# Kernel tuning notes

Hardware: AMD Instinct MI355X
Metric: run time of the kernel (lower is better)

## Reference

```python
import jax, jax.numpy as jnp
import numpy as np

B, C, S = 4, 512, 8192   # batch, channels, seq len
E = 256                  # q_dim // r1 = projected dim
D = 256                  # dilaion: block size; window width = 2*D (D even)


def setup_inputs() -> dict:
    key = jax.random.key(0)
    ks = jax.random.split(key, 6)
    w = 0.05
    return {
        "x1": jax.random.normal(ks[0], (B, C, S), jnp.float32),
        "mask": jnp.ones((B, 1, S), jnp.float32),
        "Wq": jax.random.normal(ks[1], (E, C), jnp.float32) * w,
        "bq": jnp.zeros((E,), jnp.float32),
        "Wk": jax.random.normal(ks[2], (E, C), jnp.float32) * w,
        "bk": jnp.zeros((E,), jnp.float32),
        "Wv": jax.random.normal(ks[3], (E, C), jnp.float32) * w,
        "bv": jnp.zeros((E,), jnp.float32),
        "Wo": jax.random.normal(ks[4], (C, E), jnp.float32) * w,
        "bo": jnp.zeros((C,), jnp.float32),
    }


def _windows(x, nb, d):
    # x: [B, ch, S] -> nb overlapping windows of width 2d (stride d, halo d//2 each side)
    b, ch, _ = x.shape
    xp = jnp.pad(x, ((0, 0), (0, 0), (d // 2, d // 2)))  # [B, ch, S + d]
    lo = xp[:, :, : nb * d].reshape(b, ch, nb, d)
    hi = xp[:, :, d:].reshape(b, ch, nb, d)
    return jnp.concatenate([lo, hi], axis=-1).transpose(0, 2, 1, 3)  # [B, nb, ch, 2d]


def reference(x1, mask, Wq, bq, Wk, bk, Wv, bv, Wo, bo):
    nb = S // D  # S divisible by D -> no tail padding branch
    # 1x1 conv projections
    q = jnp.einsum('ec,bcs->bes', Wq, x1) + bq[None, :, None]
    k = jnp.einsum('ec,bcs->bes', Wk, x1) + bk[None, :, None]
    v = jnp.einsum('ec,bcs->bes', Wv, x1) + bv[None, :, None]

    qw = q.reshape(B, E, nb, D).transpose(0, 2, 1, 3)   # [B, nb, E, D]
    kw = _windows(k, nb, D)                              # [B, nb, E, 2D]
    vw = _windows(v, nb, D)                              # [B, nb, E, 2D]
    pm = mask[:, 0:1, :]                                 # padding mask [B,1,S]
    pmw = _windows(pm, nb, D)                            # [B, nb, 1, 2D]

    W = 2 * D
    # original loop `window_mask[:, :, i:i+D] = 1 for i in range(D)` -> union covers
    # columns [0, 2D-2]; only the last column stays 0 (rows identical)
    win = (jnp.arange(W) < W - 1).astype(jnp.float32)    # [2D]
    fmask = win[None, None, None, :] * pmw               # [B, nb, 1, 2D]

    energy = jnp.einsum('bneq,bnek->bnqk', qw, kw) / np.float32(np.sqrt(E))
    attn = jax.nn.softmax(energy + jnp.log(fmask + 1e-6), axis=-1) * fmask
    out = jnp.einsum('bnek,bnqk->bneq', vw, attn)        # [B, nb, E, D]

    h = jax.nn.gelu(out, approximate=False)
    h = jnp.einsum('oe,bneq->bnoq', Wo, h) + bo[None, None, :, None]  # [B, nb, C, D]
    y = h.transpose(0, 2, 1, 3).reshape(B, C, nb * D)[:, :, :S]
    return y * mask[:, 0:1, :]
```

## Files before the change

### kernel.cpp

```cpp
#include <hip/hip_runtime.h>
#include <hip/hip_bf16.h>

typedef __attribute__((ext_vector_type(8))) short short8;
typedef __attribute__((ext_vector_type(4))) float f32x4;
typedef __attribute__((ext_vector_type(4))) int int4v;

#define DI __device__ __forceinline__

constexpr int Bq = 4, Cc = 512, Ss = 8192, Ee = 256;
constexpr int SP = 8448;
constexpr long XSLAB = 4194304;

DI unsigned short f2bf(float f) {
    unsigned int u = __float_as_uint(f);
    unsigned int r = u + 0x7fffu + ((u >> 16) & 1u);
    return (unsigned short)(r >> 16);
}

union U16x8 { int4v v; unsigned short u[8]; };

DI void gll16(const void* g, void* l) {
    __builtin_amdgcn_global_load_lds(
        (const __attribute__((address_space(1))) unsigned int*)g,
        (__attribute__((address_space(3))) unsigned int*)l, 16, 0, 0);
}

DI unsigned pkbf(float lo, float hi) {
    unsigned r;
    asm("v_cvt_pk_bf16_f32 %0, %1, %2" : "=v"(r) : "v"(lo), "v"(hi));
    return r;
}

DI short8 mk8(unsigned a, unsigned b, unsigned c, unsigned d) {
    int4v v; v[0] = (int)a; v[1] = (int)b; v[2] = (int)c; v[3] = (int)d;
    union { int4v i; short8 s; } U; U.i = v; return U.s;
}

DI f32x4 max4(f32x4 a, f32x4 b) {
    f32x4 r;
    r[0] = fmaxf(a[0], b[0]); r[1] = fmaxf(a[1], b[1]);
    r[2] = fmaxf(a[2], b[2]); r[3] = fmaxf(a[3], b[3]);
    return r;
}

DI float gelu_t(float x) {
    float x2 = x * x;
    float z = x * (0.7978845608f + 0.0356774081f * x2);
    float az = fabsf(z);
    float e = __expf(-2.f * az);
    float th = (1.f - e) / (1.f + e);
    th = (z < 0.f) ? -th : th;
    return 0.5f * x * (1.f + th);
}

DI int SIG(int k)  { return ((k & 4) << 2) | ((k & 24) >> 1) | (k & 3); }
DI int SIG2(int k) { return SIG(SIG(k)); }

__global__ __launch_bounds__(256) void kprep(
    const float* __restrict__ Wq, const float* __restrict__ Wk, const float* __restrict__ Wv,
    const float* __restrict__ Wo, unsigned short* __restrict__ Wqkv_b, unsigned short* __restrict__ Wo_b,
    unsigned short* __restrict__ kTp, unsigned short* __restrict__ vp)
{
    int blk = blockIdx.x, t = threadIdx.x;
    if (blk < 1536) {
        int i = blk * 256 + t;
        if (i < 768 * 512) {
            int m = i >> 9, c = i & 511;
            const float* src = (m < 256) ? Wq : ((m < 512) ? Wk : Wv);
            Wqkv_b[i] = f2bf(src[(m & 255) * 512 + c]);
        }
        if (i < 512 * 256) {
            int kap = i & 255;
            int src = (i & ~255) | (kap & ~31) | SIG(kap & 31);
            Wo_b[i] = f2bf(Wo[src]);
        }
    } else {
        int i = (blk - 1536) * 256 + t;
        int4v z = {0, 0, 0, 0};
        if (i < 32768) {
            int b = i >> 13, r = i & 8191;
            int side = r >> 12, off = r & 4095;
            *(int4v*)(kTp + (long)b * SP * 256 + (long)(side ? 8320 : 0) * 256 + off * 8) = z;
        } else {
            int j = i - 32768;
            int b = j >> 13, r = j & 8191;
            int row = r >> 5, side = (r >> 4) & 1, sc = r & 15;
            *(int4v*)(vp + ((long)b * 256 + row) * SP + side * 8320 + sc * 8) = z;
        }
    }
}

__global__ __launch_bounds__(256) void ktr_x(const float* __restrict__ x1g, unsigned short* __restrict__ xT4)
{
    const float* x1b = x1g + (long)blockIdx.y * Cc * Ss;
    unsigned short* xT = xT4 + (long)blockIdx.y * XSLAB;
    __shared__ unsigned short tile[64][72];
    int t = threadIdx.x;
    int bs = blockIdx.x & 127, bc = blockIdx.x >> 7;
    int s0 = bs * 64, c0 = bc * 64;
    int cl = t >> 4, sl = (t & 15) * 4;
    for (int it = 0; it < 4; ++it) {
        int c = cl + it * 16;
        float4 vv = *(const float4*)(x1b + (long)(c0 + c) * Ss + s0 + sl);
        tile[c][sl + 0] = f2bf(vv.x);
        tile[c][sl + 1] = f2bf(vv.y);
        tile[c][sl + 2] = f2bf(vv.z);
        tile[c][sl + 3] = f2bf(vv.w);
    }
    __syncthreads();
    int s_loc = t >> 2, cseg = (t & 3) * 16;
    for (int half = 0; half < 2; ++half) {
        U16x8 u;
        for (int j = 0; j < 8; ++j) u.u[j] = tile[cseg + half * 8 + j][s_loc];
        *(int4v*)(xT + (long)(s0 + s_loc) * Cc + c0 + cseg + half * 8) = u.v;
    }
}

__global__ __launch_bounds__(256) void kqkv(
    const unsigned short* __restrict__ xT4, const unsigned short* __restrict__ Wqkv,
    const float* __restrict__ bq, const float* __restrict__ bk, const float* __restrict__ bv,
    unsigned short* __restrict__ qT, unsigned short* __restrict__ kTp, unsigned short* __restrict__ vp,
    int b0)
{
    __shared__ int4v As[1024], Bs[1024];
    int b = b0 + blockIdx.y;
    const unsigned short* xT = xT4 + (long)blockIdx.y * XSLAB;
    int wg = blockIdx.x;
    int type = wg >> 7, id = wg & 127;
    const unsigned short *A, *Bt; unsigned short* Op;
    long opitch; const float* bias; bool biasRow;
    if (type < 2) {
        int mt = id >> 1, nt = id & 1;
        A  = xT + (long)(mt * 128) * 512;
        Bt = Wqkv + (long)(type * 256 + nt * 128) * 512;
        if (type == 0)
            Op = qT + (long)b * Ss * Ee + (long)(mt * 128) * Ee + nt * 128;
        else
            Op = kTp + (long)b * SP * Ee + (long)(128 + mt * 128) * Ee + nt * 128;
        opitch = Ee;
        bias = (type ? bk : bq) + nt * 128;
        biasRow = false;
    } else {
        int mt = id >> 6, nt = id & 63;
        A  = Wqkv + (long)(512 + mt * 128) * 512;
        Bt = xT + (long)(nt * 128) * 512;
        Op = vp + (long)b * Ee * SP + (long)(mt * 128) * SP + 128 + nt * 128;
        opitch = SP;
        bias = bv + mt * 128;
        biasRow = true;
    }
    int t = threadIdx.x, lane = t & 63, wv = t >> 6;
    int wr = (wv >> 1) * 64, wc = (wv & 1) * 64;

    int soff[4];
    #pragma unroll
    for (int i = 0; i < 4; ++i) {
        int seg = t + 256 * i, row = seg >> 3, cs = seg & 7;
        soff[i] = row * 512 + ((cs ^ (row & 7)) * 8);
    }
    char* adst = (char*)As + wv * 1024;
    char* bdst = (char*)Bs + wv * 1024;

    f32x4 acc[4][4] = {};
    for (int kk = 0; kk < 8; ++kk) {
        #pragma unroll
        for (int i = 0; i < 4; ++i) {
            gll16(A  + soff[i] + kk * 64, adst + i * 4096);
            gll16(Bt + soff[i] + kk * 64, bdst + i * 4096);
        }
        asm volatile("s_waitcnt vmcnt(0)" ::: "memory");
        __syncthreads();
        for (int ks = 0; ks < 2; ++ks) {
            int csk = ks * 4 + (lane >> 4);
            short8 af[4], bfr[4];
            #pragma unroll
            for (int mi = 0; mi < 4; ++mi) {
                int m = wr + mi * 16 + (lane & 15);
                af[mi] = *(const short8*)&As[m * 8 + (csk ^ (m & 7))];
            }
            #pragma unroll
            for (int ni = 0; ni < 4; ++ni) {
                int nn = wc + ni * 16 + (lane & 15);
                bfr[ni] = *(const short8*)&Bs[nn * 8 + (csk ^ (nn & 7))];
            }
            #pragma unroll
            for (int mi = 0; mi < 4; ++mi)
                #pragma unroll
                for (int ni = 0; ni < 4; ++ni)
                    acc[mi][ni] = __builtin_amdgcn_mfma_f32_16x16x32_bf16(af[mi], bfr[ni], acc[mi][ni], 0, 0, 0);
        }
        __syncthreads();
    }
    for (int mi = 0; mi < 4; ++mi)
        for (int ni = 0; ni < 4; ++ni) {
            int mrow = wr + mi * 16 + ((lane >> 4) * 4);
            int ncol = wc + ni * 16 + (lane & 15);
            int nc2 = biasRow ? ((ncol & ~31) | SIG2(ncol & 31)) : ncol;
            for (int r = 0; r < 4; ++r) {
                float bval = biasRow ? bias[mrow + r] : bias[ncol];
                Op[(long)(mrow + r) * opitch + nc2] = f2bf(acc[mi][ni][r] + bval);
            }
        }
}

__global__ __launch_bounds__(512, 1) void kattn(
    const unsigned short* __restrict__ qT, const unsigned short* __restrict__ kTp,
    const unsigned short* __restrict__ vp,  const unsigned short* __restrict__ Wo_b,
    const float* __restrict__ mask, const float* __restrict__ bo,
    float* __restrict__ y)
{
    __shared__ __align__(16) char SH[137216];
    float* fmaskL = (float*)(SH + 131072);
    float* lmaskL = (float*)(SH + 133120);
    float* boL    = (float*)(SH + 135168);

    int t = threadIdx.x, lane = t & 63, wv = t >> 6;
    int G = lane >> 4, l15 = lane & 15;

    int phys = blockIdx.x;
    int xx = phys & 7, kk2 = phys >> 3;
    int L = ((xx + 8 * (kk2 >> 1)) << 1) | (kk2 & 1);
    int qh = L & 1, n = (L >> 1) & 31, b = L >> 6;
    int sqw = n * 256 + qh * 128 + wv * 16;

    short8 qfrag[8];
    #pragma unroll
    for (int s = 0; s < 8; ++s)
        qfrag[s] = *(const short8*)(qT + ((long)b * Ss + sqw + l15) * 256 + 32 * s + 8 * G);

    {
        int i = t;
        int sw = n * 256 - 128 + i;
        float f = 0.f;
        if (i != 511 && sw >= 0 && sw < Ss) f = mask[(long)b * Ss + sw];
        fmaskL[i] = f;
        lmaskL[i] = __logf(f + 1e-6f);
    }
    if (t < 128) ((float4*)boL)[t] = ((const float4*)bo)[t];

    const unsigned short* ksrcp[4];
    const unsigned short* vsrcp[4];
    #pragma unroll
    for (int i = 0; i < 4; ++i) {
        int krow = wv * 8 + i * 2 + (lane >> 5);
        ksrcp[i] = kTp + ((long)b * SP + n * 256 + krow) * 256 + (((lane & 31) ^ (krow & 7)) * 8);
        int erow = wv * 32 + i * 8 + (lane >> 3);
        vsrcp[i] = vp + ((long)b * 256 + erow) * SP + n * 256 + (((lane & 7) ^ ((lane >> 3) & 7)) * 8);
    }

#define STAGE(CH, BUF) {                                                      \
        char* kl = SH + (BUF) * 32768 + wv * 4096;                            \
        char* vl = SH + 65536 + (BUF) * 32768 + wv * 4096;                    \
        _Pragma("unroll")                                                     \
        for (int i = 0; i < 4; ++i) gll16(ksrcp[i] + (long)(CH) * 16384, kl + i * 1024); \
        _Pragma("unroll")                                                     \
        for (int i = 0; i < 4; ++i) gll16(vsrcp[i] + (CH) * 64, vl + i * 1024);          \
    }

    STAGE(0, 0)
    STAGE(1, 1)
    asm volatile("s_waitcnt vmcnt(8) lgkmcnt(0)" ::: "memory");
    __builtin_amdgcn_s_barrier();

    float mrun = -1e30f, lrun = 0.f;
    f32x4 oacc[16] = {};

    for (int ch = 0; ch < 8; ++ch) {
        const char* KB = SH + (ch & 1) * 32768;
        const char* VB = SH + 65536 + (ch & 1) * 32768;

        f32x4 eacc[4] = {};
        __builtin_amdgcn_s_setprio(1);
        #pragma unroll
        for (int s = 0; s < 8; ++s) {
            short8 kf[4];
            #pragma unroll
            for (int tt = 0; tt < 4; ++tt)
                kf[tt] = *(const short8*)(KB + (16 * tt + l15) * 512 + (((4 * s + G) ^ (l15 & 7)) * 16));
            #pragma unroll
            for (int tt = 0; tt < 4; ++tt)
                eacc[tt] = __builtin_amdgcn_mfma_f32_16x16x32_bf16(kf[tt], qfrag[s], eacc[tt], 0, 0, 0);
        }
        __builtin_amdgcn_s_setprio(0);

        int w0 = ch * 64;
        f32x4 lm[4], fm[4];
        #pragma unroll
        for (int tt = 0; tt < 4; ++tt) {
            lm[tt] = *(const f32x4*)&lmaskL[w0 + 16 * tt + 4 * G];
            fm[tt] = *(const f32x4*)&fmaskL[w0 + 16 * tt + 4 * G];
        }

        f32x4 ev[4];
        f32x4 m4;
        #pragma unroll
        for (int tt = 0; tt < 4; ++tt) {
            ev[tt] = eacc[tt] * 0.0625f + lm[tt];
            m4 = tt ? max4(m4, ev[tt]) : ev[tt];
        }
        float cm = fmaxf(fmaxf(m4[0], m4[1]), fmaxf(m4[2], m4[3]));
        cm = fmaxf(cm, __shfl_xor(cm, 16));
        cm = fmaxf(cm, __shfl_xor(cm, 32));
        if (__any(cm > mrun + 8.f)) {
            float mn = fmaxf(mrun, cm);
            float sc = __expf(mrun - mn);
            mrun = mn; lrun *= sc;
            #pragma unroll
            for (int et = 0; et < 16; ++et) oacc[et] *= sc;
        }

        unsigned pc[8];
        float ssum = 0.f;
        #pragma unroll
        for (int tt = 0; tt < 4; ++tt) {
            f32x4 p;
            p[0] = __expf(ev[tt][0] - mrun);
            p[1] = __expf(ev[tt][1] - mrun);
            p[2] = __expf(ev[tt][2] - mrun);
            p[3] = __expf(ev[tt][3] - mrun);
            ssum += (p[0] + p[1]) + (p[2] + p[3]);
            f32x4 pf = p * fm[tt];
            pc[2 * tt]     = pkbf(pf[0], pf[1]);
            pc[2 * tt + 1] = pkbf(pf[2], pf[3]);
        }
        ssum += __shfl_xor(ssum, 16);
        ssum += __shfl_xor(ssum, 32);
        lrun += ssum;

        __builtin_amdgcn_s_setprio(1);
        #pragma unroll
        for (int s = 0; s < 2; ++s) {
            short8 pf = mk8(pc[4 * s], pc[4 * s + 1], pc[4 * s + 2], pc[4 * s + 3]);
            #pragma unroll
            for (int et = 0; et < 16; ++et) {
                short8 vf = *(const short8*)(VB + (16 * et + l15) * 128 + (((4 * s + G) ^ (l15 & 7)) * 16));
                oacc[et] = __builtin_amdgcn_mfma_f32_16x16x32_bf16(vf, pf, oacc[et], 0, 0, 0);
            }
        }
        __builtin_amdgcn_s_setprio(0);

        asm volatile("s_waitcnt lgkmcnt(0)" ::: "memory");
        __builtin_amdgcn_s_barrier();
        if (ch < 6) {
            STAGE(ch + 2, ch & 1)
            asm volatile("s_waitcnt vmcnt(8)" ::: "memory");
        } else if (ch == 6) {
            asm volatile("s_waitcnt vmcnt(0)" ::: "memory");
        }
        __builtin_amdgcn_s_barrier();
    }

    float linv = 1.f / lrun;
    unsigned hc[32];
    #pragma unroll
    for (int et = 0; et < 16; ++et) {
        f32x4 xv = oacc[et] * linv;
        hc[2 * et]     = pkbf(gelu_t(xv[0]), gelu_t(xv[1]));
        hc[2 * et + 1] = pkbf(gelu_t(xv[2]), gelu_t(xv[3]));
    }
    float ym = fmaskL[128 + qh * 128 + wv * 16 + l15];

    const unsigned short* wsrcp[4];
    #pragma unroll
    for (int i = 0; i < 4; ++i) {
        int wrow = wv * 8 + i * 2 + (lane >> 5);
        wsrcp[i] = Wo_b + (long)wrow * 256 + (((lane & 31) ^ (wrow & 7)) * 8);
    }
#define WSTAGE(ST, BUF) {                                                     \
        char* wl = SH + (BUF) * 32768 + wv * 4096;                            \
        _Pragma("unroll")                                                     \
        for (int i = 0; i < 4; ++i) gll16(wsrcp[i] + (ST) * 16384, wl + i * 1024); \
    }

    WSTAGE(0, 0)
    WSTAGE(1, 1)
    asm volatile("s_waitcnt vmcnt(4)" ::: "memory");
    __builtin_amdgcn_s_barrier();

    for (int step = 0; step < 8; ++step) {
        const char* WB = SH + (step & 1) * 32768;
        __builtin_amdgcn_s_setprio(1);
        #pragma unroll
        for (int otl = 0; otl < 4; ++otl) {
            f32x4 pacc = {};
            #pragma unroll
            for (int s = 0; s < 8; ++s) {
                short8 wf = *(const short8*)(WB + (16 * otl + l15) * 512 + (((4 * s + G) ^ (l15 & 7)) * 16));
                short8 hs = mk8(hc[4 * s], hc[4 * s + 1], hc[4 * s + 2], hc[4 * s + 3]);
                pacc = __builtin_amdgcn_mfma_f32_16x16x32_bf16(wf, hs, pacc, 0, 0, 0);
            }
            int o0 = step * 64 + 16 * otl + 4 * G;
            f32x4 bo4 = *(const f32x4*)&boL[o0];
            #pragma unroll
            for (int r = 0; r < 4; ++r)
                y[((long)b * Cc + o0 + r) * Ss + sqw + l15] = (pacc[r] + bo4[r]) * ym;
        }
        __builtin_amdgcn_s_setprio(0);
        asm volatile("s_waitcnt lgkmcnt(0)" ::: "memory");
        __builtin_amdgcn_s_barrier();
        if (step < 6) {
            WSTAGE(step + 2, step & 1)
            asm volatile("s_waitcnt vmcnt(4)" ::: "memory");
        } else if (step == 6) {
            asm volatile("s_waitcnt vmcnt(0)" ::: "memory");
        }
        __builtin_amdgcn_s_barrier();
    }
#undef STAGE
#undef WSTAGE
}

extern "C" void kernel_launch(void* const* d_in, const int* in_sizes, int n_in,
                              void* d_out, int out_size, void* d_ws, size_t ws_size,
                              hipStream_t stream)
{
    const float* x1   = (const float*)d_in[0];
    const float* mask = (const float*)d_in[1];
    const float* Wq   = (const float*)d_in[2];
    const float* bq   = (const float*)d_in[3];
    const float* Wk   = (const float*)d_in[4];
    const float* bk   = (const float*)d_in[5];
    const float* Wv   = (const float*)d_in[6];
    const float* bv   = (const float*)d_in[7];
    const float* Wo   = (const float*)d_in[8];
    const float* bo   = (const float*)d_in[9];
    float* y = (float*)d_out;

    if (ws_size < 60817408u) return;
    char* w = (char*)d_ws;
    unsigned short* Wqkv_b = (unsigned short*)(w);
    unsigned short* Wo_b   = (unsigned short*)(w + 786432);
    unsigned short* qT     = (unsigned short*)(w + 1048576);
    unsigned short* kTp    = (unsigned short*)(w + 17825792);
    unsigned short* vp     = (unsigned short*)(w + 35127296);
    unsigned short* xT4    = (unsigned short*)(w + 52428800);

    int g = (int)((ws_size - 52428800u) / 8388608u);
    if (g < 1) g = 1;
    if (g > 4) g = 4;

    kprep<<<1792, 256, 0, stream>>>(Wq, Wk, Wv, Wo, Wqkv_b, Wo_b, kTp, vp);
    for (int b0 = 0; b0 < 4; b0 += g) {
        int gy = (4 - b0 < g) ? (4 - b0) : g;
        ktr_x<<<dim3(1024, gy), 256, 0, stream>>>(x1 + (long)b0 * Cc * Ss, xT4);
        kqkv<<<dim3(384, gy), 256, 0, stream>>>(xT4, Wqkv_b, bq, bk, bv, qT, kTp, vp, b0);
    }
    kattn<<<256, 512, 0, stream>>>(qT, kTp, vp, Wo_b, mask, bo, y);
}
```

Before: 118.9 us.

## Software-pipeline QK^T one chunk ahead and switch softmax to exp2

Computes the QK energy MFMA block for chunk ch+1 before the softmax and PV work of chunk ch, so matrix ops can overlap the exp/max reductions. The K+V staging wait is tightened (vmcnt 8 to 4) so the next chunk's K is ready earlier. The softmax moves to base 2 by folding log2(e) into the scale and storing the mask log in base 2, which avoids an extra multiply per exp. It costs a second set of energy accumulators, which raises register pressure, and the waits become stricter.

```diff
diff --git a/kernel.cpp b/kernel.cpp
--- a/kernel.cpp
+++ b/kernel.cpp
@@ -211,7 +211,7 @@
 {
     __shared__ __align__(16) char SH[137216];
     float* fmaskL = (float*)(SH + 131072);
-    float* lmaskL = (float*)(SH + 133120);
+    float* l2maskL = (float*)(SH + 133120);
     float* boL    = (float*)(SH + 135168);
 
     int t = threadIdx.x, lane = t & 63, wv = t >> 6;
@@ -234,7 +234,7 @@
         float f = 0.f;
         if (i != 511 && sw >= 0 && sw < Ss) f = mask[(long)b * Ss + sw];
         fmaskL[i] = f;
-        lmaskL[i] = __logf(f + 1e-6f);
+        l2maskL[i] = __log2f(f + 1e-6f);
     }
     if (t < 128) ((float4*)boL)[t] = ((const float4*)bo)[t];
 
@@ -257,37 +257,46 @@
         for (int i = 0; i < 4; ++i) gll16(vsrcp[i] + (CH) * 64, vl + i * 1024);          \
     }
 
+#define QKBLOCK(E, KB) {                                                      \
+        __builtin_amdgcn_s_setprio(1);                                        \
+        _Pragma("unroll")                                                     \
+        for (int s = 0; s < 8; ++s) {                                         \
+            short8 kf[4];                                                     \
+            _Pragma("unroll")                                                 \
+            for (int tt = 0; tt < 4; ++tt)                                    \
+                kf[tt] = *(const short8*)((KB) + (16 * tt + l15) * 512 + (((4 * s + G) ^ (l15 & 7)) * 16)); \
+            _Pragma("unroll")                                                 \
+            for (int tt = 0; tt < 4; ++tt)                                    \
+                E[tt] = __builtin_amdgcn_mfma_f32_16x16x32_bf16(kf[tt], qfrag[s], E[tt], 0, 0, 0); \
+        }                                                                     \
+        __builtin_amdgcn_s_setprio(0);                                        \
+    }
+
     STAGE(0, 0)
     STAGE(1, 1)
-    asm volatile("s_waitcnt vmcnt(8) lgkmcnt(0)" ::: "memory");
+    asm volatile("s_waitcnt vmcnt(4) lgkmcnt(0)" ::: "memory");
     __builtin_amdgcn_s_barrier();
 
     float mrun = -1e30f, lrun = 0.f;
     f32x4 oacc[16] = {};
-
+    f32x4 eC[4] = {}, eN[4] = {};
+
+    QKBLOCK(eC, SH)
+
+    #pragma unroll 2
     for (int ch = 0; ch < 8; ++ch) {
-        const char* KB = SH + (ch & 1) * 32768;
         const char* VB = SH + 65536 + (ch & 1) * 32768;
 
-        f32x4 eacc[4] = {};
-        __builtin_amdgcn_s_setprio(1);
-        #pragma unroll
-        for (int s = 0; s < 8; ++s) {
-            short8 kf[4];
-            #pragma unroll
-            for (int tt = 0; tt < 4; ++tt)
-                kf[tt] = *(const short8*)(KB + (16 * tt + l15) * 512 + (((4 * s + G) ^ (l15 & 7)) * 16));
-            #pragma unroll
-            for (int tt = 0; tt < 4; ++tt)
-                eacc[tt] = __builtin_amdgcn_mfma_f32_16x16x32_bf16(kf[tt], qfrag[s], eacc[tt], 0, 0, 0);
-        }
-        __builtin_amdgcn_s_setprio(0);
+        if (ch < 7) {
+            const char* KBn = SH + ((ch + 1) & 1) * 32768;
+            QKBLOCK(eN, KBn)
+        }
 
         int w0 = ch * 64;
         f32x4 lm[4], fm[4];
         #pragma unroll
         for (int tt = 0; tt < 4; ++tt) {
-            lm[tt] = *(const f32x4*)&lmaskL[w0 + 16 * tt + 4 * G];
+            lm[tt] = *(const f32x4*)&l2maskL[w0 + 16 * tt + 4 * G];
             fm[tt] = *(const f32x4*)&fmaskL[w0 + 16 * tt + 4 * G];
         }
 
@@ -295,15 +304,15 @@
         f32x4 m4;
         #pragma unroll
         for (int tt = 0; tt < 4; ++tt) {
-            ev[tt] = eacc[tt] * 0.0625f + lm[tt];
+            ev[tt] = eC[tt] * 0.09016844f + lm[tt];
             m4 = tt ? max4(m4, ev[tt]) : ev[tt];
         }
         float cm = fmaxf(fmaxf(m4[0], m4[1]), fmaxf(m4[2], m4[3]));
         cm = fmaxf(cm, __shfl_xor(cm, 16));
         cm = fmaxf(cm, __shfl_xor(cm, 32));
-        if (__any(cm > mrun + 8.f)) {
+        if (__any(cm > mrun + 11.5416f)) {
             float mn = fmaxf(mrun, cm);
-            float sc = __expf(mrun - mn);
+            float sc = exp2f(mrun - mn);
             mrun = mn; lrun *= sc;
             #pragma unroll
             for (int et = 0; et < 16; ++et) oacc[et] *= sc;
@@ -314,10 +323,10 @@
         #pragma unroll
         for (int tt = 0; tt < 4; ++tt) {
             f32x4 p;
-            p[0] = __expf(ev[tt][0] - mrun);
-            p[1] = __expf(ev[tt][1] - mrun);
-            p[2] = __expf(ev[tt][2] - mrun);
-            p[3] = __expf(ev[tt][3] - mrun);
+            p[0] = exp2f(ev[tt][0] - mrun);
+            p[1] = exp2f(ev[tt][1] - mrun);
+            p[2] = exp2f(ev[tt][2] - mrun);
+            p[3] = exp2f(ev[tt][3] - mrun);
             ssum += (p[0] + p[1]) + (p[2] + p[3]);
             f32x4 pf = p * fm[tt];
             pc[2 * tt]     = pkbf(pf[0], pf[1]);
@@ -343,11 +352,14 @@
         __builtin_amdgcn_s_barrier();
         if (ch < 6) {
             STAGE(ch + 2, ch & 1)
-            asm volatile("s_waitcnt vmcnt(8)" ::: "memory");
+            asm volatile("s_waitcnt vmcnt(4)" ::: "memory");
         } else if (ch == 6) {
             asm volatile("s_waitcnt vmcnt(0)" ::: "memory");
         }
         __builtin_amdgcn_s_barrier();
+
+        #pragma unroll
+        for (int tt = 0; tt < 4; ++tt) { eC[tt] = eN[tt]; eN[tt] = (f32x4){}; }
     }
 
     float linv = 1.f / lrun;
@@ -408,6 +420,7 @@
     }
 #undef STAGE
 #undef WSTAGE
+#undef QKBLOCK
 }
 
 extern "C" void kernel_launch(void* const* d_in, const int* in_sizes, int n_in,
```

New measurement: 122.8 us. 1.03x slower.

## Fuse x transpose into prep kernel, stage xT in output buffer, use exp2 softmax

Applied to the files above, without the earlier changes.

Merges the x1 bf16 transpose into the weight-prep kernel and launches a single qkv GEMM over all batches, storing the transposed activations in the output buffer instead of a workspace slab. This removes several kernel launches and the batch-group loop. Softmax now works in base 2 with a folded scale and log2 mask, so exp2 replaces __expf, and the first Wo tile is prefetched during the last attention chunk. Reusing d_out as scratch depends on kattn fully overwriting y after kqkv has finished reading xT, which stream ordering provides.

```diff
diff --git a/kernel.cpp b/kernel.cpp
--- a/kernel.cpp
+++ b/kernel.cpp
@@ -56,14 +56,39 @@
 DI int SIG(int k)  { return ((k & 4) << 2) | ((k & 24) >> 1) | (k & 3); }
 DI int SIG2(int k) { return SIG(SIG(k)); }
 
-__global__ __launch_bounds__(256) void kprep(
+__global__ __launch_bounds__(256) void kpre(
+    const float* __restrict__ x1,
     const float* __restrict__ Wq, const float* __restrict__ Wk, const float* __restrict__ Wv,
     const float* __restrict__ Wo, unsigned short* __restrict__ Wqkv_b, unsigned short* __restrict__ Wo_b,
-    unsigned short* __restrict__ kTp, unsigned short* __restrict__ vp)
+    unsigned short* __restrict__ kTp, unsigned short* __restrict__ vp,
+    unsigned short* __restrict__ xTo)
 {
     int blk = blockIdx.x, t = threadIdx.x;
-    if (blk < 1536) {
-        int i = blk * 256 + t;
+    if (blk < 4096) {
+        int bb = blk >> 10, inner = blk & 1023;
+        const float* x1b = x1 + (long)bb * Cc * Ss;
+        unsigned short* xT = xTo + (long)bb * XSLAB;
+        __shared__ unsigned short tile[64][72];
+        int bs = inner & 127, bc = inner >> 7;
+        int s0 = bs * 64, c0 = bc * 64;
+        int cl = t >> 4, sl = (t & 15) * 4;
+        for (int it = 0; it < 4; ++it) {
+            int c = cl + it * 16;
+            float4 vv = *(const float4*)(x1b + (long)(c0 + c) * Ss + s0 + sl);
+            tile[c][sl + 0] = f2bf(vv.x);
+            tile[c][sl + 1] = f2bf(vv.y);
+            tile[c][sl + 2] = f2bf(vv.z);
+            tile[c][sl + 3] = f2bf(vv.w);
+        }
+        __syncthreads();
+        int s_loc = t >> 2, cseg = (t & 3) * 16;
+        for (int half = 0; half < 2; ++half) {
+            U16x8 u;
+            for (int j = 0; j < 8; ++j) u.u[j] = tile[cseg + half * 8 + j][s_loc];
+            *(int4v*)(xT + (long)(s0 + s_loc) * Cc + c0 + cseg + half * 8) = u.v;
+        }
+    } else if (blk < 5632) {
+        int i = (blk - 4096) * 256 + t;
         if (i < 768 * 512) {
             int m = i >> 9, c = i & 511;
             const float* src = (m < 256) ? Wq : ((m < 512) ? Wk : Wv);
@@ -75,7 +100,7 @@
             Wo_b[i] = f2bf(Wo[src]);
         }
     } else {
-        int i = (blk - 1536) * 256 + t;
+        int i = (blk - 5632) * 256 + t;
         int4v z = {0, 0, 0, 0};
         if (i < 32768) {
             int b = i >> 13, r = i & 8191;
@@ -90,41 +115,14 @@
     }
 }
 
-__global__ __launch_bounds__(256) void ktr_x(const float* __restrict__ x1g, unsigned short* __restrict__ xT4)
-{
-    const float* x1b = x1g + (long)blockIdx.y * Cc * Ss;
-    unsigned short* xT = xT4 + (long)blockIdx.y * XSLAB;
-    __shared__ unsigned short tile[64][72];
-    int t = threadIdx.x;
-    int bs = blockIdx.x & 127, bc = blockIdx.x >> 7;
-    int s0 = bs * 64, c0 = bc * 64;
-    int cl = t >> 4, sl = (t & 15) * 4;
-    for (int it = 0; it < 4; ++it) {
-        int c = cl + it * 16;
-        float4 vv = *(const float4*)(x1b + (long)(c0 + c) * Ss + s0 + sl);
-        tile[c][sl + 0] = f2bf(vv.x);
-        tile[c][sl + 1] = f2bf(vv.y);
-        tile[c][sl + 2] = f2bf(vv.z);
-        tile[c][sl + 3] = f2bf(vv.w);
-    }
-    __syncthreads();
-    int s_loc = t >> 2, cseg = (t & 3) * 16;
-    for (int half = 0; half < 2; ++half) {
-        U16x8 u;
-        for (int j = 0; j < 8; ++j) u.u[j] = tile[cseg + half * 8 + j][s_loc];
-        *(int4v*)(xT + (long)(s0 + s_loc) * Cc + c0 + cseg + half * 8) = u.v;
-    }
-}
-
 __global__ __launch_bounds__(256) void kqkv(
     const unsigned short* __restrict__ xT4, const unsigned short* __restrict__ Wqkv,
     const float* __restrict__ bq, const float* __restrict__ bk, const float* __restrict__ bv,
-    unsigned short* __restrict__ qT, unsigned short* __restrict__ kTp, unsigned short* __restrict__ vp,
-    int b0)
+    unsigned short* __restrict__ qT, unsigned short* __restrict__ kTp, unsigned short* __restrict__ vp)
 {
     __shared__ int4v As[1024], Bs[1024];
-    int b = b0 + blockIdx.y;
-    const unsigned short* xT = xT4 + (long)blockIdx.y * XSLAB;
+    int b = blockIdx.y;
+    const unsigned short* xT = xT4 + (long)b * XSLAB;
     int wg = blockIdx.x;
     int type = wg >> 7, id = wg & 127;
     const unsigned short *A, *Bt; unsigned short* Op;
@@ -210,9 +208,9 @@
     float* __restrict__ y)
 {
     __shared__ __align__(16) char SH[137216];
-    float* fmaskL = (float*)(SH + 131072);
-    float* lmaskL = (float*)(SH + 133120);
-    float* boL    = (float*)(SH + 135168);
+    float* fmaskL  = (float*)(SH + 131072);
+    float* l2maskL = (float*)(SH + 133120);
+    float* boL     = (float*)(SH + 135168);
 
     int t = threadIdx.x, lane = t & 63, wv = t >> 6;
     int G = lane >> 4, l15 = lane & 15;
@@ -234,7 +232,7 @@
         float f = 0.f;
         if (i != 511 && sw >= 0 && sw < Ss) f = mask[(long)b * Ss + sw];
         fmaskL[i] = f;
-        lmaskL[i] = __logf(f + 1e-6f);
+        l2maskL[i] = __log2f(f + 1e-6f);
     }
     if (t < 128) ((float4*)boL)[t] = ((const float4*)bo)[t];
 
@@ -247,6 +245,12 @@
         int erow = wv * 32 + i * 8 + (lane >> 3);
         vsrcp[i] = vp + ((long)b * 256 + erow) * SP + n * 256 + (((lane & 7) ^ ((lane >> 3) & 7)) * 8);
     }
+    const unsigned short* wsrcp[4];
+    #pragma unroll
+    for (int i = 0; i < 4; ++i) {
+        int wrow = wv * 8 + i * 2 + (lane >> 5);
+        wsrcp[i] = Wo_b + (long)wrow * 256 + (((lane & 31) ^ (wrow & 7)) * 8);
+    }
 
 #define STAGE(CH, BUF) {                                                      \
         char* kl = SH + (BUF) * 32768 + wv * 4096;                            \
@@ -256,6 +260,11 @@
         _Pragma("unroll")                                                     \
         for (int i = 0; i < 4; ++i) gll16(vsrcp[i] + (CH) * 64, vl + i * 1024);          \
     }
+#define WSTAGE(ST, BUF) {                                                     \
+        char* wl = SH + (BUF) * 32768 + wv * 4096;                            \
+        _Pragma("unroll")                                                     \
+        for (int i = 0; i < 4; ++i) gll16(wsrcp[i] + (ST) * 16384, wl + i * 1024); \
+    }
 
     STAGE(0, 0)
     STAGE(1, 1)
@@ -287,7 +296,7 @@
         f32x4 lm[4], fm[4];
         #pragma unroll
         for (int tt = 0; tt < 4; ++tt) {
-            lm[tt] = *(const f32x4*)&lmaskL[w0 + 16 * tt + 4 * G];
+            lm[tt] = *(const f32x4*)&l2maskL[w0 + 16 * tt + 4 * G];
             fm[tt] = *(const f32x4*)&fmaskL[w0 + 16 * tt + 4 * G];
         }
 
@@ -295,15 +304,15 @@
         f32x4 m4;
         #pragma unroll
         for (int tt = 0; tt < 4; ++tt) {
-            ev[tt] = eacc[tt] * 0.0625f + lm[tt];
+            ev[tt] = eacc[tt] * 0.09016844f + lm[tt];
             m4 = tt ? max4(m4, ev[tt]) : ev[tt];
         }
         float cm = fmaxf(fmaxf(m4[0], m4[1]), fmaxf(m4[2], m4[3]));
         cm = fmaxf(cm, __shfl_xor(cm, 16));
         cm = fmaxf(cm, __shfl_xor(cm, 32));
-        if (__any(cm > mrun + 8.f)) {
+        if (__any(cm > mrun + 11.5416f)) {
             float mn = fmaxf(mrun, cm);
-            float sc = __expf(mrun - mn);
+            float sc = exp2f(mrun - mn);
             mrun = mn; lrun *= sc;
             #pragma unroll
             for (int et = 0; et < 16; ++et) oacc[et] *= sc;
@@ -314,10 +323,10 @@
         #pragma unroll
         for (int tt = 0; tt < 4; ++tt) {
             f32x4 p;
-            p[0] = __expf(ev[tt][0] - mrun);
-            p[1] = __expf(ev[tt][1] - mrun);
-            p[2] = __expf(ev[tt][2] - mrun);
-            p[3] = __expf(ev[tt][3] - mrun);
+            p[0] = exp2f(ev[tt][0] - mrun);
+            p[1] = exp2f(ev[tt][1] - mrun);
+            p[2] = exp2f(ev[tt][2] - mrun);
+            p[3] = exp2f(ev[tt][3] - mrun);
             ssum += (p[0] + p[1]) + (p[2] + p[3]);
             f32x4 pf = p * fm[tt];
             pc[2 * tt]     = pkbf(pf[0], pf[1]);
@@ -345,7 +354,8 @@
             STAGE(ch + 2, ch & 1)
             asm volatile("s_waitcnt vmcnt(8)" ::: "memory");
         } else if (ch == 6) {
-            asm volatile("s_waitcnt vmcnt(0)" ::: "memory");
+            WSTAGE(0, 0)
+            asm volatile("s_waitcnt vmcnt(4)" ::: "memory");
         }
         __builtin_amdgcn_s_barrier();
     }
@@ -360,19 +370,6 @@
     }
     float ym = fmaskL[128 + qh * 128 + wv * 16 + l15];
 
-    const unsigned short* wsrcp[4];
-    #pragma unroll
-    for (int i = 0; i < 4; ++i) {
-        int wrow = wv * 8 + i * 2 + (lane >> 5);
-        wsrcp[i] = Wo_b + (long)wrow * 256 + (((lane & 31) ^ (wrow & 7)) * 8);
-    }
-#define WSTAGE(ST, BUF) {                                                     \
-        char* wl = SH + (BUF) * 32768 + wv * 4096;                            \
-        _Pragma("unroll")                                                     \
-        for (int i = 0; i < 4; ++i) gll16(wsrcp[i] + (ST) * 16384, wl + i * 1024); \
-    }
-
-    WSTAGE(0, 0)
     WSTAGE(1, 1)
     asm volatile("s_waitcnt vmcnt(4)" ::: "memory");
     __builtin_amdgcn_s_barrier();
@@ -426,24 +423,16 @@
     const float* bo   = (const float*)d_in[9];
     float* y = (float*)d_out;
 
-    if (ws_size < 60817408u) return;
+    if (ws_size < 52428800u) return;
     char* w = (char*)d_ws;
     unsigned short* Wqkv_b = (unsigned short*)(w);
     unsigned short* Wo_b   = (unsigned short*)(w + 786432);
     unsigned short* qT     = (unsigned short*)(w + 1048576);
     unsigned short* kTp    = (unsigned short*)(w + 17825792);
     unsigned short* vp     = (unsigned short*)(w + 35127296);
-    unsigned short* xT4    = (unsigned short*)(w + 52428800);
-
-    int g = (int)((ws_size - 52428800u) / 8388608u);
-    if (g < 1) g = 1;
-    if (g > 4) g = 4;
-
-    kprep<<<1792, 256, 0, stream>>>(Wq, Wk, Wv, Wo, Wqkv_b, Wo_b, kTp, vp);
-    for (int b0 = 0; b0 < 4; b0 += g) {
-        int gy = (4 - b0 < g) ? (4 - b0) : g;
-        ktr_x<<<dim3(1024, gy), 256, 0, stream>>>(x1 + (long)b0 * Cc * Ss, xT4);
-        kqkv<<<dim3(384, gy), 256, 0, stream>>>(xT4, Wqkv_b, bq, bk, bv, qT, kTp, vp, b0);
-    }
+    unsigned short* xT4    = (unsigned short*)d_out;
+
+    kpre<<<5888, 256, 0, stream>>>(x1, Wq, Wk, Wv, Wo, Wqkv_b, Wo_b, kTp, vp, xT4);
+    kqkv<<<dim3(384, 4), 256, 0, stream>>>(xT4, Wqkv_b, bq, bk, bv, qT, kTp, vp);
     kattn<<<256, 512, 0, stream>>>(qT, kTp, vp, Wo_b, mask, bo, y);
 }
```

New measurement: 116.3 us. 2.2% less time.
